# Optimization experiments

Hardware: AMD Instinct MI355X
Metric: run time of the kernel (lower is better)

Reference implementation:

```python
import jax, jax.numpy as jnp
import numpy as np

B, T, C, H = 4, 1024, 1024, 16
D = C // H


def setup_inputs() -> dict:
    key = jax.random.key(0)
    ks = jax.random.split(key, 6)
    s = 1.0 / np.sqrt(C)
    return {
        "x": jax.random.normal(ks[0], (B, T, C), jnp.float32),
        "W_qkv": jax.random.normal(ks[1], (C, 3 * C), jnp.float32) * s,
        "b_qkv": jnp.zeros((3 * C,), jnp.float32),
        "W_out": jax.random.normal(ks[2], (C, C), jnp.float32) * s,
        "b_out": jnp.zeros((C,), jnp.float32),
        "w_sur": jax.random.normal(ks[3], (C,), jnp.float32) * s,
        "b_sur": jnp.zeros((), jnp.float32),
        "threshold": jnp.float32(0.5),
    }


def _expmap0_split(u):
    # geoopt Lorentz (k=1) expmap0: first coordinate is the time axis.
    # Minkowski norm of tangent u: sqrt(clamp(-u0^2 + |u_rest|^2, 1e-8))
    mink = -u[..., :1] ** 2 + jnp.sum(u[..., 1:] ** 2, axis=-1, keepdims=True)
    nomin = jnp.sqrt(jnp.maximum(mink, 1e-8))  # [..., 1]
    time = jnp.cosh(nomin)                      # [..., 1]
    space = jnp.sinh(nomin) * u[..., 1:] / nomin  # [..., D-1]
    return time, space


def reference(x, W_qkv, b_qkv, W_out, b_out, w_sur, b_sur, threshold):
    Bx, Tx, Cx = x.shape
    # spiking gate on query rows (causal tril over a (T,1) matrix is all-True -> no-op)
    importance = jax.nn.sigmoid(jnp.einsum("btc,c->bt", x, w_sur) + b_sur)  # [B,T]
    spikes = (importance > threshold).astype(x.dtype)                       # [B,T]
    spike_mask = spikes[:, None, :, None]                                   # [B,1,T,1]

    qkv = x @ W_qkv + b_qkv                                                 # [B,T,3C]
    qkv = qkv.reshape(Bx, Tx, 3, H, D).transpose(2, 0, 3, 1, 4)             # [3,B,H,T,D]
    q, k, v = qkv[0], qkv[1], qkv[2]

    tq, sq = _expmap0_split(q)  # [B,H,T,1], [B,H,T,D-1]
    tk, sk = _expmap0_split(k)
    # -<x,y>_L = tq*tk - <sq,sk>  (pairwise, via matmuls instead of broadcast tensors)
    neg_inner = jnp.einsum("bhie,bhje->bhij", tq, tk) - jnp.einsum(
        "bhid,bhjd->bhij", sq, sk
    )  # [B,H,T,T]
    dist = jnp.arccosh(jnp.maximum(neg_inner, 1.0 + 1e-7))
    scores = -(dist ** 2) / np.sqrt(D)

    causal = jnp.tril(jnp.ones((Tx, Tx), dtype=bool))
    scores = jnp.where(causal[None, None], scores, -jnp.inf)
    attn = jax.nn.softmax(scores, axis=-1) * spike_mask                     # [B,H,T,T]

    y = jnp.einsum("bhij,bhjd->bhid", attn, v)                              # [B,H,T,D]
    y = y.transpose(0, 2, 1, 3).reshape(Bx, Tx, Cx)
    return y @ W_out + b_out
```

## Files before the change

kernel.cpp:

```cpp
#include <hip/hip_runtime.h>
#include <math.h>

#define BB 4
#define TT 1024
#define CC 1024
#define HH 16
#define DD 64
#define NQKV (3 * CC)
#define MROWS (BB * TT)

typedef __attribute__((ext_vector_type(8))) short bf16x8;
typedef __attribute__((ext_vector_type(4))) float f32x4;

struct alignas(8) US4 { unsigned short x, y, z, w; };

__device__ __forceinline__ float b2f(unsigned short u) {
  unsigned int w = ((unsigned int)u) << 16;
  float f; __builtin_memcpy(&f, &w, 4); return f;
}
__device__ __forceinline__ unsigned short f2b(float f) {
  unsigned int u; __builtin_memcpy(&u, &f, 4);
  u += 0x7FFFu + ((u >> 16) & 1);
  return (unsigned short)(u >> 16);
}

__device__ __forceinline__ void gload16(const void* g, void* l) {
  __builtin_amdgcn_global_load_lds(
      (const __attribute__((address_space(1))) unsigned int*)g,
      (__attribute__((address_space(3))) unsigned int*)l, 16, 0, 0);
}

__device__ __forceinline__ bf16x8 ld_sw(const unsigned short* row_base,
                                        int lc, int rsw) {
  return *(const bf16x8*)((const char*)row_base + (((lc ^ rsw) & 7) << 4));
}

__global__ __launch_bounds__(256) void prep(
    const float* __restrict__ x, const float* __restrict__ w_sur,
    const float* __restrict__ b_sur, const float* __restrict__ thr,
    const float* __restrict__ W_qkv, const float* __restrict__ W_out,
    float* __restrict__ spikes, unsigned short* __restrict__ xb,
    unsigned short* __restrict__ WqkvT, unsigned short* __restrict__ WoutT) {
  __shared__ float t[32][33];
  const int blk = blockIdx.x;

  if (blk < 4096) {
    const float* W; unsigned short* WT; int K, N, bx, by;
    if (blk < 3072) {
      W = W_qkv; WT = WqkvT; K = CC; N = NQKV;
      bx = blk % 96; by = blk / 96;
    } else {
      W = W_out; WT = WoutT; K = CC; N = CC;
      const int b2 = blk - 3072;
      bx = b2 & 31; by = b2 >> 5;
    }
    const int tx = threadIdx.x & 31, ty = threadIdx.x >> 5;
    const int k0 = by * 32, n0 = bx * 32;
#pragma unroll
    for (int i = 0; i < 32; i += 8)
      t[ty + i][tx] = W[(size_t)(k0 + ty + i) * N + n0 + tx];
    __syncthreads();
#pragma unroll
    for (int i = 0; i < 32; i += 8)
      WT[(size_t)(n0 + ty + i) * K + k0 + tx] = f2b(t[tx][ty + i]);
  } else {
    const int row = (blk - 4096) * 4 + (threadIdx.x >> 6);
    const int lane = threadIdx.x & 63;
    const float* xr = x + (size_t)row * CC;
    unsigned short* xo = xb + (size_t)row * CC;
    double acc = 0.0;
#pragma unroll
    for (int s = 0; s < 4; ++s) {
      const int idx = s * 256 + lane * 4;
      const float4 xv = *(const float4*)(xr + idx);
      const float4 wv = *(const float4*)(w_sur + idx);
      acc += (double)xv.x * (double)wv.x;
      acc += (double)xv.y * (double)wv.y;
      acc += (double)xv.z * (double)wv.z;
      acc += (double)xv.w * (double)wv.w;
      US4 o = {f2b(xv.x), f2b(xv.y), f2b(xv.z), f2b(xv.w)};
      *(US4*)(xo + idx) = o;
    }
#pragma unroll
    for (int off = 32; off > 0; off >>= 1) acc += __shfl_xor(acc, off, 64);
    if (lane == 0) {
      const float z = (float)acc + b_sur[0];
      const float imp = 1.0f / (1.0f + __expf(-z));
      spikes[row] = (imp > thr[0]) ? 1.0f : 0.0f;
    }
  }
}

__global__ __launch_bounds__(256) void gemm_qkv(
    const unsigned short* __restrict__ A, const unsigned short* __restrict__ BT,
    const float* __restrict__ bias, unsigned short* __restrict__ qkvb,
    unsigned short* __restrict__ vT) {
  const int K = CC;
  __shared__ unsigned short SH[12288];
  unsigned short (*As)[64] = (unsigned short(*)[64])SH;
  unsigned short (*Bs)[64] = (unsigned short(*)[64])(SH + 8192);
  const int tid = threadIdx.x;
  const int lane = tid & 63;
  const int wave = tid >> 6;
  const int wm = wave * 32;
  const int m0 = blockIdx.y * 128;
  const int n0 = blockIdx.x * 64;
  const int ln15 = lane & 15;
  const int g = lane >> 4;
  const int rsw = ln15 & 7;

  const int srow = tid >> 3;
  const int schk = ((tid & 7) ^ (srow & 7)) * 8;
  const unsigned short* gA = A + (size_t)(m0 + srow) * K + schk;
  const unsigned short* gB = BT + (size_t)(n0 + srow) * K + schk;
  char* lA = (char*)SH + wave * 1024;
  char* lB = (char*)SH + 16384 + wave * 1024;

  f32x4 acc[2][4] = {};

  for (int k0 = 0; k0 < K; k0 += 64) {
    __syncthreads();
#pragma unroll
    for (int i = 0; i < 4; ++i)
      gload16(gA + k0 + (size_t)(32 * i) * K, lA + i * 4096);
#pragma unroll
    for (int i = 0; i < 2; ++i)
      gload16(gB + k0 + (size_t)(32 * i) * K, lB + i * 4096);
    __syncthreads();

#pragma unroll
    for (int c = 0; c < 2; ++c) {
      bf16x8 af[2], bfr[4];
#pragma unroll
      for (int i = 0; i < 2; ++i)
        af[i] = ld_sw(&As[wm + i * 16 + ln15][0], c * 4 + g, rsw);
#pragma unroll
      for (int j = 0; j < 4; ++j)
        bfr[j] = ld_sw(&Bs[j * 16 + ln15][0], c * 4 + g, rsw);
#pragma unroll
      for (int i = 0; i < 2; ++i)
#pragma unroll
        for (int j = 0; j < 4; ++j)
          acc[i][j] = __builtin_amdgcn_mfma_f32_16x16x32_bf16(
              af[i], bfr[j], acc[i][j], 0, 0, 0);
    }
  }

  __syncthreads();
  unsigned short* scr = SH + wave * 2048;

  const int bx = blockIdx.x;
  if (bx < 32) {
    const bool isk = (bx >= 16);
#pragma unroll
    for (int i = 0; i < 2; ++i) {
#pragma unroll
      for (int r = 0; r < 4; ++r) {
        float u[4];
        float part = 0.f;
#pragma unroll
        for (int j = 0; j < 4; ++j) {
          u[j] = acc[i][j][r] + bias[n0 + j * 16 + ln15];
          float sq = u[j] * u[j];
          if (j == 0 && ln15 == 0) sq = -sq;
          part += sq;
        }
#pragma unroll
        for (int off = 1; off < 16; off <<= 1)
          part += __shfl_xor(part, off, 64);
        const float nomin = sqrtf(fmaxf(part, 1e-8f));
        const float e = __expf(nomin);
        const float ei = __builtin_amdgcn_rcpf(e);
        const float tim = 0.5f * (e + ei);
        const float coef = 0.5f * (e - ei) * __builtin_amdgcn_rcpf(nomin);
        const int lrow = i * 16 + g * 4 + r;
#pragma unroll
        for (int j = 0; j < 4; ++j) {
          float o = (j == 0 && ln15 == 0) ? tim : coef * u[j];
          if (isk && !(j == 0 && ln15 == 0)) o = -o;
          const int col = j * 16 + ln15;
          const int ch = ((col >> 3) + lrow) & 7;
          scr[lrow * 64 + ch * 8 + (col & 7)] = f2b(o);
        }
      }
    }
#pragma unroll
    for (int it = 0; it < 4; ++it) {
      const int row = (lane >> 3) + 8 * it;
      const int ch = lane & 7;
      const int ph = (ch + row) & 7;
      const bf16x8 v = *(const bf16x8*)&scr[row * 64 + ph * 8];
      *(bf16x8*)&qkvb[(size_t)(m0 + wm + row) * NQKV + n0 + ch * 8] = v;
    }
  } else {
#pragma unroll
    for (int i = 0; i < 2; ++i) {
#pragma unroll
      for (int j = 0; j < 4; ++j) {
        const float bb_ = bias[n0 + j * 16 + ln15];
        const int drow = j * 16 + ln15;
#pragma unroll
        for (int r = 0; r < 4; ++r) {
          const int col = i * 16 + g * 4 + r;
          const int ch = ((col >> 3) + drow) & 3;
          scr[drow * 32 + ch * 8 + (col & 7)] = f2b(acc[i][j][r] + bb_);
        }
      }
    }
    const int hh = bx - 32;
    const int mbase = m0 + wm;
    const int bq = mbase >> 10;
    const int t0 = mbase & 1023;
#pragma unroll
    for (int it = 0; it < 4; ++it) {
      const int drow = (lane >> 2) + 16 * it;
      const int ch = lane & 3;
      const int ph = (ch + drow) & 3;
      const bf16x8 v = *(const bf16x8*)&scr[drow * 32 + ph * 8];
      *(bf16x8*)&vT[((size_t)(bq * HH + hh) * DD + drow) * TT + t0 + ch * 8] = v;
    }
  }
}

__global__ __launch_bounds__(256) void gemm_out(
    const unsigned short* __restrict__ A, const unsigned short* __restrict__ BT,
    const float* __restrict__ bias, float* __restrict__ C) {
  const int N = CC, K = CC;
  __shared__ unsigned short As[128][64];
  __shared__ unsigned short Bs[64][64];
  const int tid = threadIdx.x;
  const int lane = tid & 63;
  const int wave = tid >> 6;
  const int wm = wave * 32;
  const int m0 = blockIdx.y * 128;
  const int n0 = blockIdx.x * 64;
  const int ln15 = lane & 15;
  const int g = lane >> 4;
  const int rsw = ln15 & 7;

  const int srow = tid >> 3;
  const int schk = ((tid & 7) ^ (srow & 7)) * 8;
  const unsigned short* gA = A + (size_t)(m0 + srow) * K + schk;
  const unsigned short* gB = BT + (size_t)(n0 + srow) * K + schk;
  char* lA = (char*)As + wave * 1024;
  char* lB = (char*)Bs + wave * 1024;

  f32x4 acc[2][4] = {};

  for (int k0 = 0; k0 < K; k0 += 64) {
    __syncthreads();
#pragma unroll
    for (int i = 0; i < 4; ++i)
      gload16(gA + k0 + (size_t)(32 * i) * K, lA + i * 4096);
#pragma unroll
    for (int i = 0; i < 2; ++i)
      gload16(gB + k0 + (size_t)(32 * i) * K, lB + i * 4096);
    __syncthreads();

#pragma unroll
    for (int c = 0; c < 2; ++c) {
      bf16x8 af[2], bfr[4];
#pragma unroll
      for (int i = 0; i < 2; ++i)
        af[i] = ld_sw(&As[wm + i * 16 + ln15][0], c * 4 + g, rsw);
#pragma unroll
      for (int j = 0; j < 4; ++j)
        bfr[j] = ld_sw(&Bs[j * 16 + ln15][0], c * 4 + g, rsw);
#pragma unroll
      for (int i = 0; i < 2; ++i)
#pragma unroll
        for (int j = 0; j < 4; ++j)
          acc[i][j] = __builtin_amdgcn_mfma_f32_16x16x32_bf16(
              af[i], bfr[j], acc[i][j], 0, 0, 0);
    }
  }

#pragma unroll
  for (int i = 0; i < 2; ++i) {
#pragma unroll
    for (int r = 0; r < 4; ++r) {
      const int m = m0 + wm + i * 16 + g * 4 + r;
#pragma unroll
      for (int j = 0; j < 4; ++j) {
        const int n = n0 + j * 16 + ln15;
        C[(size_t)m * N + n] = acc[i][j][r] + bias[n];
      }
    }
  }
}

__global__ __launch_bounds__(512) void flash_mfma(
    const unsigned short* __restrict__ qkv, const unsigned short* __restrict__ vT,
    const float* __restrict__ spikes, unsigned short* __restrict__ y) {
  __shared__ unsigned short Ks[64][68];
  __shared__ unsigned short Vs[64][68];
  __shared__ unsigned short Ps[128][68];

  const int tid = threadIdx.x;
  const int lane = tid & 63;
  const int wave = tid >> 6;
  const int ln15 = lane & 15;
  const int g = lane >> 4;
  const int bh = blockIdx.y;
  const int itile = (bh < 32) ? ((int)gridDim.x - 1 - (int)blockIdx.x)
                              : (int)blockIdx.x;
  const int b = bh >> 4;
  const int h = bh & 15;
  const int i0 = itile * 128;
  const int band = wave * 16;
  const int ntiles = 2 * itile + 2;
  const unsigned short* base = qkv + (size_t)b * TT * NQKV;
  const unsigned short* vbase = vT + (size_t)bh * DD * TT;
  const int qoff = h * DD;
  const int koff = CC + h * DD;

  const int sn = tid >> 3;
  const int qc = tid & 7;

  bf16x8 qf[2];
  {
    const unsigned short* qp = base + (size_t)(i0 + band + ln15) * NQKV + qoff;
    qf[0] = *(const bf16x8*)(qp + g * 8);
    qf[1] = *(const bf16x8*)(qp + 32 + g * 8);
  }

  f32x4 accy[4] = {};
  float lrow[4] = {0.f, 0.f, 0.f, 0.f};

  float4 kr, vr;
  {
    const unsigned short* kp = base + (size_t)sn * NQKV + koff + qc * 8;
    const unsigned short* vp = vbase + (size_t)sn * TT + qc * 8;
    kr = *(const float4*)kp;
    vr = *(const float4*)vp;
  }

  for (int jt = 0; jt < ntiles; ++jt) {
    const int j0 = jt * 64;
    __syncthreads();
    *(float4*)&Ks[sn][qc * 8] = kr;
    *(float4*)&Vs[sn][qc * 8] = vr;
    __syncthreads();

    if (jt + 1 < ntiles) {
      const int j1 = j0 + 64;
      const unsigned short* kp = base + (size_t)(j1 + sn) * NQKV + koff + qc * 8;
      const unsigned short* vp = vbase + (size_t)sn * TT + j1 + qc * 8;
      kr = *(const float4*)kp;
      vr = *(const float4*)vp;
    }

    if (j0 > i0 + band + 15) continue;

    f32x4 sf[4];
#pragma unroll
    for (int j = 0; j < 4; ++j) {
      const bf16x8 k0 = *(const bf16x8*)&Ks[j * 16 + ln15][g * 8];
      const bf16x8 k1 = *(const bf16x8*)&Ks[j * 16 + ln15][32 + g * 8];
      f32x4 z = {};
      z = __builtin_amdgcn_mfma_f32_16x16x32_bf16(qf[0], k0, z, 0, 0, 0);
      sf[j] = __builtin_amdgcn_mfma_f32_16x16x32_bf16(qf[1], k1, z, 0, 0, 0);
    }

    float p[4][4];
#pragma unroll
    for (int j = 0; j < 4; ++j) {
      const int gj = j0 + j * 16 + ln15;
#pragma unroll
      for (int r = 0; r < 4; ++r) {
        const int gi = i0 + band + g * 4 + r;
        float e;
        if (gj > gi) {
          e = 0.f;
        } else {
          const float lnz = __logf(fmaxf(sf[j][r], 1.0f));
          const float s = fmaf(lnz, 1.44269504f, 1.0f);
          e = __expf(-0.06005663f * s * s);
        }
        p[r][j] = e;
      }
    }
#pragma unroll
    for (int r = 0; r < 4; ++r)
      lrow[r] += (p[r][0] + p[r][1]) + (p[r][2] + p[r][3]);

#pragma unroll
    for (int r = 0; r < 4; ++r)
#pragma unroll
      for (int j = 0; j < 4; ++j)
        Ps[band + g * 4 + r][j * 16 + ln15] = f2b(p[r][j]);

    const bf16x8 pa0 = *(const bf16x8*)&Ps[band + ln15][g * 8];
    const bf16x8 pa1 = *(const bf16x8*)&Ps[band + ln15][32 + g * 8];
#pragma unroll
    for (int dt = 0; dt < 4; ++dt) {
      const bf16x8 v0 = *(const bf16x8*)&Vs[dt * 16 + ln15][g * 8];
      const bf16x8 v1 = *(const bf16x8*)&Vs[dt * 16 + ln15][32 + g * 8];
      accy[dt] = __builtin_amdgcn_mfma_f32_16x16x32_bf16(pa0, v0, accy[dt], 0, 0, 0);
      accy[dt] = __builtin_amdgcn_mfma_f32_16x16x32_bf16(pa1, v1, accy[dt], 0, 0, 0);
    }
  }

#pragma unroll
  for (int r = 0; r < 4; ++r) {
#pragma unroll
    for (int off = 1; off < 16; off <<= 1)
      lrow[r] += __shfl_xor(lrow[r], off, 64);
  }
  const int grow = b * TT + i0 + band + g * 4;
#pragma unroll
  for (int r = 0; r < 4; ++r) {
    const float spk = spikes[grow + r];
    const float scale = spk / lrow[r];
#pragma unroll
    for (int dt = 0; dt < 4; ++dt)
      y[(size_t)(grow + r) * CC + h * DD + dt * 16 + ln15] =
          f2b(accy[dt][r] * scale);
  }
}

extern "C" void kernel_launch(void* const* d_in, const int* in_sizes, int n_in,
                              void* d_out, int out_size, void* d_ws, size_t ws_size,
                              hipStream_t stream) {
  const float* x     = (const float*)d_in[0];
  const float* W_qkv = (const float*)d_in[1];
  const float* b_qkv = (const float*)d_in[2];
  const float* W_out = (const float*)d_in[3];
  const float* b_out = (const float*)d_in[4];
  const float* w_sur = (const float*)d_in[5];
  const float* b_sur = (const float*)d_in[6];
  const float* thr   = (const float*)d_in[7];
  float* out = (float*)d_out;

  char* w = (char*)d_ws;
  unsigned short* xb    = (unsigned short*)(w);
  unsigned short* qkvb  = (unsigned short*)(w + 8388608);
  unsigned short* vTb   = (unsigned short*)(w + 8388608 + 25165824);
  unsigned short* ybufb = (unsigned short*)(w + 8388608 + 25165824 + 8388608);
  unsigned short* WqkvT = (unsigned short*)(w + 8388608 + 25165824 + 2 * 8388608);
  unsigned short* WoutT = (unsigned short*)(w + 8388608 + 25165824 + 2 * 8388608 + 6291456);
  float* spikes = (float*)(w + 8388608 + 25165824 + 2 * 8388608 + 6291456 + 2097152);

  prep<<<5120, 256, 0, stream>>>(x, w_sur, b_sur, thr, W_qkv, W_out,
                                 spikes, xb, WqkvT, WoutT);

  gemm_qkv<<<dim3(NQKV / 64, MROWS / 128), 256, 0, stream>>>(
      xb, WqkvT, b_qkv, qkvb, vTb);

  flash_mfma<<<dim3(TT / 128, BB * HH), 512, 0, stream>>>(qkvb, vTb, spikes, ybufb);

  gemm_out<<<dim3(CC / 64, MROWS / 128), 256, 0, stream>>>(
      ybufb, WoutT, b_out, out);
}
```

Baseline: 181.9 us.

## Stage 128-key tiles per barrier, use hw log2/exp2, skip masking on full tiles

The flash attention loop now loads 128 keys/values into shared memory per iteration and processes them as two 64-key subtiles, which halves the number of block-wide barriers and global load rounds. The log/exp in the score transform are replaced with the hardware log2/exp2 builtins, with the constants folded so the result is unchanged. Fully unmasked subtiles skip the per-element causal comparison. Shared memory use grows, and one extra 64-key half tile of loading may be wasted on the diagonal.

```diff
diff --git a/kernel.cpp b/kernel.cpp
--- a/kernel.cpp
+++ b/kernel.cpp
@@ -22,6 +22,13 @@
   unsigned int u; __builtin_memcpy(&u, &f, 4);
   u += 0x7FFFu + ((u >> 16) & 1);
   return (unsigned short)(u >> 16);
+}
+
+__device__ __forceinline__ float hw_log2(float x) {
+  return __builtin_amdgcn_logf(x);
+}
+__device__ __forceinline__ float hw_exp2(float x) {
+  return __builtin_amdgcn_exp2f(x);
 }
 
 __device__ __forceinline__ void gload16(const void* g, void* l) {
@@ -292,8 +299,8 @@
 __global__ __launch_bounds__(512) void flash_mfma(
     const unsigned short* __restrict__ qkv, const unsigned short* __restrict__ vT,
     const float* __restrict__ spikes, unsigned short* __restrict__ y) {
-  __shared__ unsigned short Ks[64][68];
-  __shared__ unsigned short Vs[64][68];
+  __shared__ unsigned short Ks[128][68];
+  __shared__ unsigned short Vs[64][136];
   __shared__ unsigned short Ps[128][68];
 
   const int tid = threadIdx.x;
@@ -308,14 +315,16 @@
   const int h = bh & 15;
   const int i0 = itile * 128;
   const int band = wave * 16;
-  const int ntiles = 2 * itile + 2;
+  const int htiles = itile + 1;
   const unsigned short* base = qkv + (size_t)b * TT * NQKV;
   const unsigned short* vbase = vT + (size_t)bh * DD * TT;
   const int qoff = h * DD;
   const int koff = CC + h * DD;
 
-  const int sn = tid >> 3;
-  const int qc = tid & 7;
+  const int ksn = tid >> 2;
+  const int kqc = (tid & 3) * 2;
+  const int vsn = tid >> 3;
+  const int vqc = (tid & 7) * 2;
 
   bf16x8 qf[2];
   {
@@ -327,77 +336,98 @@
   f32x4 accy[4] = {};
   float lrow[4] = {0.f, 0.f, 0.f, 0.f};
 
-  float4 kr, vr;
+  float4 kr0, kr1, vr0, vr1;
   {
-    const unsigned short* kp = base + (size_t)sn * NQKV + koff + qc * 8;
-    const unsigned short* vp = vbase + (size_t)sn * TT + qc * 8;
-    kr = *(const float4*)kp;
-    vr = *(const float4*)vp;
-  }
-
-  for (int jt = 0; jt < ntiles; ++jt) {
-    const int j0 = jt * 64;
-    __syncthreads();
-    *(float4*)&Ks[sn][qc * 8] = kr;
-    *(float4*)&Vs[sn][qc * 8] = vr;
-    __syncthreads();
-
-    if (jt + 1 < ntiles) {
-      const int j1 = j0 + 64;
-      const unsigned short* kp = base + (size_t)(j1 + sn) * NQKV + koff + qc * 8;
-      const unsigned short* vp = vbase + (size_t)sn * TT + j1 + qc * 8;
-      kr = *(const float4*)kp;
-      vr = *(const float4*)vp;
-    }
-
-    if (j0 > i0 + band + 15) continue;
-
-    f32x4 sf[4];
-#pragma unroll
-    for (int j = 0; j < 4; ++j) {
-      const bf16x8 k0 = *(const bf16x8*)&Ks[j * 16 + ln15][g * 8];
-      const bf16x8 k1 = *(const bf16x8*)&Ks[j * 16 + ln15][32 + g * 8];
-      f32x4 z = {};
-      z = __builtin_amdgcn_mfma_f32_16x16x32_bf16(qf[0], k0, z, 0, 0, 0);
-      sf[j] = __builtin_amdgcn_mfma_f32_16x16x32_bf16(qf[1], k1, z, 0, 0, 0);
-    }
-
-    float p[4][4];
-#pragma unroll
-    for (int j = 0; j < 4; ++j) {
-      const int gj = j0 + j * 16 + ln15;
-#pragma unroll
-      for (int r = 0; r < 4; ++r) {
-        const int gi = i0 + band + g * 4 + r;
-        float e;
-        if (gj > gi) {
-          e = 0.f;
-        } else {
-          const float lnz = __logf(fmaxf(sf[j][r], 1.0f));
-          const float s = fmaf(lnz, 1.44269504f, 1.0f);
-          e = __expf(-0.06005663f * s * s);
+    const unsigned short* kp = base + (size_t)ksn * NQKV + koff + kqc * 8;
+    const unsigned short* vp = vbase + (size_t)vsn * TT + vqc * 8;
+    kr0 = *(const float4*)(kp + 0);
+    kr1 = *(const float4*)(kp + 8);
+    vr0 = *(const float4*)(vp + 0);
+    vr1 = *(const float4*)(vp + 8);
+  }
+
+  for (int ht = 0; ht < htiles; ++ht) {
+    const int j0h = ht * 128;
+    __syncthreads();
+    *(float4*)&Ks[ksn][kqc * 8 + 0] = kr0;
+    *(float4*)&Ks[ksn][kqc * 8 + 8] = kr1;
+    *(float4*)&Vs[vsn][vqc * 8 + 0] = vr0;
+    *(float4*)&Vs[vsn][vqc * 8 + 8] = vr1;
+    __syncthreads();
+
+    if (ht + 1 < htiles) {
+      const int j1 = j0h + 128;
+      const unsigned short* kp = base + (size_t)(j1 + ksn) * NQKV + koff + kqc * 8;
+      const unsigned short* vp = vbase + (size_t)vsn * TT + j1 + vqc * 8;
+      kr0 = *(const float4*)(kp + 0);
+      kr1 = *(const float4*)(kp + 8);
+      vr0 = *(const float4*)(vp + 0);
+      vr1 = *(const float4*)(vp + 8);
+    }
+
+#pragma unroll
+    for (int t2 = 0; t2 < 2; ++t2) {
+      const int j0 = j0h + t2 * 64;
+      if (j0 > i0 + band + 15) continue;
+
+      f32x4 sf[4];
+#pragma unroll
+      for (int j = 0; j < 4; ++j) {
+        const bf16x8 k0 = *(const bf16x8*)&Ks[t2 * 64 + j * 16 + ln15][g * 8];
+        const bf16x8 k1 = *(const bf16x8*)&Ks[t2 * 64 + j * 16 + ln15][32 + g * 8];
+        f32x4 z = {};
+        z = __builtin_amdgcn_mfma_f32_16x16x32_bf16(qf[0], k0, z, 0, 0, 0);
+        sf[j] = __builtin_amdgcn_mfma_f32_16x16x32_bf16(qf[1], k1, z, 0, 0, 0);
+      }
+
+      float p[4][4];
+      if (j0 + 63 <= i0 + band) {
+#pragma unroll
+        for (int j = 0; j < 4; ++j)
+#pragma unroll
+          for (int r = 0; r < 4; ++r) {
+            const float l = hw_log2(fmaxf(sf[j][r], 1.0f));
+            const float s = l + 1.0f;
+            p[r][j] = hw_exp2(-0.08664339757f * s * s);
+          }
+      } else {
+#pragma unroll
+        for (int j = 0; j < 4; ++j) {
+          const int gj = j0 + j * 16 + ln15;
+#pragma unroll
+          for (int r = 0; r < 4; ++r) {
+            const int gi = i0 + band + g * 4 + r;
+            float e;
+            if (gj > gi) {
+              e = 0.f;
+            } else {
+              const float l = hw_log2(fmaxf(sf[j][r], 1.0f));
+              const float s = l + 1.0f;
+              e = hw_exp2(-0.08664339757f * s * s);
+            }
+            p[r][j] = e;
+          }
         }
-        p[r][j] = e;
-      }
-    }
-#pragma unroll
-    for (int r = 0; r < 4; ++r)
-      lrow[r] += (p[r][0] + p[r][1]) + (p[r][2] + p[r][3]);
-
-#pragma unroll
-    for (int r = 0; r < 4; ++r)
-#pragma unroll
-      for (int j = 0; j < 4; ++j)
-        Ps[band + g * 4 + r][j * 16 + ln15] = f2b(p[r][j]);
-
-    const bf16x8 pa0 = *(const bf16x8*)&Ps[band + ln15][g * 8];
-    const bf16x8 pa1 = *(const bf16x8*)&Ps[band + ln15][32 + g * 8];
-#pragma unroll
-    for (int dt = 0; dt < 4; ++dt) {
-      const bf16x8 v0 = *(const bf16x8*)&Vs[dt * 16 + ln15][g * 8];
-      const bf16x8 v1 = *(const bf16x8*)&Vs[dt * 16 + ln15][32 + g * 8];
-      accy[dt] = __builtin_amdgcn_mfma_f32_16x16x32_bf16(pa0, v0, accy[dt], 0, 0, 0);
-      accy[dt] = __builtin_amdgcn_mfma_f32_16x16x32_bf16(pa1, v1, accy[dt], 0, 0, 0);
+      }
+#pragma unroll
+      for (int r = 0; r < 4; ++r)
+        lrow[r] += (p[r][0] + p[r][1]) + (p[r][2] + p[r][3]);
+
+#pragma unroll
+      for (int r = 0; r < 4; ++r)
+#pragma unroll
+        for (int j = 0; j < 4; ++j)
+          Ps[band + g * 4 + r][j * 16 + ln15] = f2b(p[r][j]);
+
+      const bf16x8 pa0 = *(const bf16x8*)&Ps[band + ln15][g * 8];
+      const bf16x8 pa1 = *(const bf16x8*)&Ps[band + ln15][32 + g * 8];
+#pragma unroll
+      for (int dt = 0; dt < 4; ++dt) {
+        const bf16x8 v0 = *(const bf16x8*)&Vs[dt * 16 + ln15][t2 * 64 + g * 8];
+        const bf16x8 v1 = *(const bf16x8*)&Vs[dt * 16 + ln15][t2 * 64 + 32 + g * 8];
+        accy[dt] = __builtin_amdgcn_mfma_f32_16x16x32_bf16(pa0, v0, accy[dt], 0, 0, 0);
+        accy[dt] = __builtin_amdgcn_mfma_f32_16x16x32_bf16(pa1, v1, accy[dt], 0, 0, 0);
+      }
     }
   }
 
```

New measurement: 172.8 us. -5.0%, faster.
